# Optimization experiments

Hardware: AMD Instinct MI355X
Metric: run time of the kernel (lower is better)

Reference implementation:

```python
import jax, jax.numpy as jnp
import numpy as np


def _unfold(x, r):
    # x: [b, ch, h, w] -> [b, ch, k*k, h, w], zero-padded 3x3-style neighborhoods
    b, ch, h, w = x.shape
    k = 2 * r + 1
    xp = jnp.pad(x, ((0, 0), (0, 0), (r, r), (r, r)))
    patches = [xp[:, :, i:i + h, j:j + w] for i in range(k) for j in range(k)]
    return jnp.stack(patches, axis=2)


def setup_inputs() -> dict:
    key = jax.random.key(0)
    ks = jax.random.split(key, 6)
    b, c, h, w = 4, 128, 128, 128
    scale = 1.0 / np.sqrt(c)
    return {
        "feature0": jax.random.normal(ks[0], (b, c, h, w), jnp.float32),
        "flow": jax.random.normal(ks[1], (b, 2, h, w), jnp.float32),
        "q_w": jax.random.normal(ks[2], (c, c), jnp.float32) * scale,
        "q_b": jax.random.normal(ks[3], (c,), jnp.float32) * 0.01,
        "k_w": jax.random.normal(ks[4], (c, c), jnp.float32) * scale,
        "k_b": jax.random.normal(ks[5], (c,), jnp.float32) * 0.01,
        "local_window_attn": 1,
        "local_window_radius": 1,
    }


def reference(feature0, flow, q_w, q_b, k_w, k_b, local_window_attn, local_window_radius):
    b, c, h, w = feature0.shape
    inv_sqrt_c = 1.0 / jnp.sqrt(jnp.asarray(c, feature0.dtype))
    x = feature0.reshape(b, c, h * w).transpose(0, 2, 1)  # [b, hw, c]
    q = x @ q_w.T + q_b  # q_proj
    if local_window_attn:
        r = local_window_radius
        kf = x @ k_w.T + k_b  # k_proj applied to original feature
        kmap = kf.transpose(0, 2, 1).reshape(b, c, h, w)
        kwin = _unfold(kmap, r)      # [b, c, k2, h, w]
        fwin = _unfold(flow, r)      # [b, 2, k2, h, w]
        qmap = q.reshape(b, h, w, c)
        scores = jnp.einsum('bhwc,bckhw->bhwk', qmap, kwin) * inv_sqrt_c
        prob = jax.nn.softmax(scores, axis=-1)
        out = jnp.einsum('bhwk,bfkhw->bfhw', prob, fwin)  # [b, 2, h, w]
        return out
    else:
        # NOTE: faithful to source, key = k_proj(q_proj(x))
        key_ = q @ k_w.T + k_b
        value = flow.reshape(b, flow.shape[1], h * w).transpose(0, 2, 1)  # [b, hw, 2]
        scores = jnp.einsum('bnc,bmc->bnm', q, key_) * inv_sqrt_c
        prob = jax.nn.softmax(scores, axis=-1)
        out = jnp.einsum('bnm,bmf->bnf', prob, value)
        return out.reshape(b, h, w, value.shape[-1]).transpose(0, 3, 1, 2)
```

## Files before the change

kernel.cpp:

```cpp
#include <hip/hip_runtime.h>


#define HW 16384
#define NB 4
#define TOT (NB * HW)

typedef short bf16x8 __attribute__((ext_vector_type(8)));
typedef float f32x4 __attribute__((ext_vector_type(4)));

__device__ __forceinline__ unsigned short f2bf(float f) {
    unsigned u = __float_as_uint(f);
    return (unsigned short)((u + 0x7fffu + ((u >> 16) & 1u)) >> 16);
}
__device__ __forceinline__ float bf2f(unsigned short s) {
    return __uint_as_float(((unsigned)s) << 16);
}

__global__ void prep_kernel(const float* __restrict__ qw, const float* __restrict__ qb,
                            const float* __restrict__ kw, const float* __restrict__ kb,
                            unsigned short* __restrict__ MhT, unsigned short* __restrict__ MlT,
                            float* __restrict__ u, float* __restrict__ v,
                            float* __restrict__ dptr) {
    __shared__ float red[128];
    int bid = blockIdx.x, tid = threadIdx.x;
    if (bid < 128) {
        int ci = bid;
        int cj = tid & 127, half = tid >> 7;
        int co0 = half * 64;
        const float* kcol = kw + ci;
        float acc = 0.f;
#pragma unroll 4
        for (int co = 0; co < 64; ++co)
            acc += kcol[(size_t)(co0 + co) * 128] * qw[(size_t)(co0 + co) * 128 + cj];
        if (half) red[cj] = acc;
        __syncthreads();
        if (!half) {
            float mval = acc + red[cj];
            unsigned short h = f2bf(mval);
            MhT[ci * 128 + cj] = h;
            MlT[ci * 128 + cj] = f2bf(mval - bf2f(h));
        }
    } else {
        int half = tid >> 7, t = tid & 127;
        const float* w  = half ? kw : qw;
        const float* bv = half ? qb : kb;
        float acc = 0.f;
#pragma unroll 4
        for (int co = 0; co < 128; ++co) acc += w[co * 128 + t] * bv[co];
        if (half) v[t] = acc; else u[t] = acc;
        if (!half) red[t] = qb[t] * kb[t];
        __syncthreads();
        if (tid == 0) {
            float dd = 0.f;
            for (int i = 0; i < 128; ++i) dd += red[i];
            *dptr = dd;
        }
    }
}

__global__ __launch_bounds__(512, 4)
void fused_kernel(const float* __restrict__ feat,
                  const unsigned short* __restrict__ MhT, const unsigned short* __restrict__ MlT,
                  const float* __restrict__ u, const float* __restrict__ v,
                  const float* __restrict__ dptr, const float* __restrict__ flow,
                  float* __restrict__ out) {
    __shared__ float zbuf[16384];
    int tid = threadIdx.x;
    int bid = blockIdx.x;
    int b = bid >> 7, row = bid & 127;
    int p0 = row * 128;

    {
        char* lbase = (char*)zbuf;
#pragma unroll
        for (int it = 0; it < 4; ++it) {
            int chunk = it * 512 + tid;
            int off = chunk * 16;
            int swz = off ^ (((off >> 8) & 7) << 4);
            bf16x8 tv = *(const bf16x8*)((const char*)MhT + off);
            *(bf16x8*)(lbase + swz) = tv;
            bf16x8 tv2 = *(const bf16x8*)((const char*)MlT + off);
            *(bf16x8*)(lbase + 32768 + swz) = tv2;
        }
    }
    __syncthreads();

    {
        int wave = tid >> 6, lane = tid & 63;
        int m = lane & 15, q = lane >> 4;
        int wp0 = wave * 16;
        const float* xbase = feat + (size_t)b * 128 * HW + p0 + wp0;
        const char* lbase = (const char*)zbuf;

        f32x4 zero = {0.f, 0.f, 0.f, 0.f};
        f32x4 acc[8];
#pragma unroll
        for (int t = 0; t < 8; ++t) acc[t] = zero;

#pragma unroll
        for (int kc = 0; kc < 4; ++kc) {
            int c0 = kc * 32;
            const float* xp = xbase + (size_t)(c0 + q * 8) * HW + m;
            float xv[8];
#pragma unroll
            for (int j = 0; j < 8; ++j) xv[j] = xp[(size_t)j * HW];
            bf16x8 bh, bl;
#pragma unroll
            for (int j = 0; j < 8; ++j) {
                unsigned short hh = f2bf(xv[j]);
                bh[j] = (short)hh;
                bl[j] = (short)f2bf(xv[j] - bf2f(hh));
            }
            int colb = (c0 + q * 8) * 2;
            int swzx = ((m & 7) << 4);
#pragma unroll
            for (int t = 0; t < 8; ++t) {
                int offr = ((t * 16 + m) * 256 + colb) ^ swzx;
                bf16x8 ah = *(const bf16x8*)(lbase + offr);
                bf16x8 al = *(const bf16x8*)(lbase + 32768 + offr);
                acc[t] = __builtin_amdgcn_mfma_f32_16x16x32_bf16(ah, bh, acc[t], 0, 0, 0);
                acc[t] = __builtin_amdgcn_mfma_f32_16x16x32_bf16(ah, bl, acc[t], 0, 0, 0);
                acc[t] = __builtin_amdgcn_mfma_f32_16x16x32_bf16(al, bh, acc[t], 0, 0, 0);
            }
        }
        __syncthreads();
        int px = wp0 + (lane & 15);
        int rg = lane >> 4;
#pragma unroll
        for (int t = 0; t < 8; ++t)
#pragma unroll
            for (int r = 0; r < 4; ++r) {
                int c = t * 16 + rg * 4 + r;
                zbuf[px * 128 + ((c + px) & 127)] = acc[t][r] + v[c];
            }
    }
    __syncthreads();

    {
        int spx = tid & 127, h = tid >> 7;
        int p = p0 + spx;
        float sc[9];
#pragma unroll
        for (int k = 0; k < 9; ++k) sc[k] = 0.f;
        float g = 0.f;
#pragma unroll 2
        for (int cc = 0; cc < 32; ++cc) {
            int c = h * 32 + cc;
            float zv = zbuf[spx * 128 + ((c + spx) & 127)];
            const float* xc = feat + ((size_t)b * 128 + c) * HW;
            float xcen = 0.f;
#pragma unroll
            for (int dy = 0; dy < 3; ++dy) {
                int off = p + (dy - 1) * 128;
                int om = max(0, min(HW - 1, off - 1));
                int oc = max(0, min(HW - 1, off));
                int op = max(0, min(HW - 1, off + 1));
                float xm = xc[om], x0 = xc[oc], xp1 = xc[op];
                sc[dy * 3 + 0] += zv * xm;
                sc[dy * 3 + 1] += zv * x0;
                sc[dy * 3 + 2] += zv * xp1;
                if (dy == 1) xcen = x0;
            }
            g += u[c] * xcen;
        }
        __syncthreads();
#pragma unroll
        for (int k = 0; k < 9; ++k)
            zbuf[(k * 128 + spx) * 4 + h] = sc[k];
        zbuf[(9 * 128 + spx) * 4 + h] = g;
    }
    __syncthreads();

    if (tid < 128) {
        int spx = tid;
        int p = p0 + spx;
        int col = spx;
        const float inv = 0.08838834764831845f;
        float dconst = *dptr;
        float g = zbuf[(9 * 128 + spx) * 4 + 0] + zbuf[(9 * 128 + spx) * 4 + 1]
                + zbuf[(9 * 128 + spx) * 4 + 2] + zbuf[(9 * 128 + spx) * 4 + 3];

        float sc[9];
        float mx = -1e30f;
#pragma unroll
        for (int k = 0; k < 9; ++k) {
            int dy = k / 3 - 1, dx = (k % 3) - 1;
            float ssum = zbuf[(k * 128 + spx) * 4 + 0] + zbuf[(k * 128 + spx) * 4 + 1]
                       + zbuf[(k * 128 + spx) * 4 + 2] + zbuf[(k * 128 + spx) * 4 + 3];
            bool valid = ((unsigned)(row + dy) < 128u) && ((unsigned)(col + dx) < 128u);
            float s = valid ? (ssum + g + dconst) * inv : 0.f;
            sc[k] = s;
            mx = fmaxf(mx, s);
        }
        float e[9], sum = 0.f;
#pragma unroll
        for (int k = 0; k < 9; ++k) { e[k] = __expf(sc[k] - mx); sum += e[k]; }
        float rs = 1.f / sum;

        float o0 = 0.f, o1 = 0.f;
#pragma unroll
        for (int k = 0; k < 9; ++k) {
            int dy = k / 3 - 1, dx = (k % 3) - 1;
            bool valid = ((unsigned)(row + dy) < 128u) && ((unsigned)(col + dx) < 128u);
            float pr = valid ? e[k] * rs : 0.f;
            int poff = p + dy * 128 + dx;
            poff = max(0, min(HW - 1, poff));
            o0 += pr * flow[(size_t)(b * 2) * HW + poff];
            o1 += pr * flow[(size_t)(b * 2 + 1) * HW + poff];
        }
        out[(size_t)(b * 2) * HW + p] = o0;
        out[(size_t)(b * 2 + 1) * HW + p] = o1;
    }
}

extern "C" void kernel_launch(void* const* d_in, const int* in_sizes, int n_in,
                              void* d_out, int out_size, void* d_ws, size_t ws_size,
                              hipStream_t stream) {
    const float* feat = (const float*)d_in[0];
    const float* flow = (const float*)d_in[1];
    const float* qw = (const float*)d_in[2];
    const float* qb = (const float*)d_in[3];
    const float* kw = (const float*)d_in[4];
    const float* kb = (const float*)d_in[5];

    float* ws = (float*)d_ws;
    float* u = ws;
    float* v = ws + 128;
    float* dptr = ws + 256;
    unsigned short* MhT = (unsigned short*)(ws + 512);
    unsigned short* MlT = (unsigned short*)(ws + 8704);
    float* out = (float*)d_out;

    prep_kernel<<<129, 256, 0, stream>>>(qw, qb, kw, kb, MhT, MlT, u, v, dptr);
    fused_kernel<<<512, 512, 0, stream>>>(feat, MhT, MlT, u, v, dptr, flow, out);
}
```

Baseline: 116.6 us.

## Consume MFMA accumulators directly for window dot products, reduce via wave shuffles

```diff
diff --git a/kernel.cpp b/kernel.cpp
--- a/kernel.cpp
+++ b/kernel.cpp
@@ -64,152 +64,148 @@
                   const float* __restrict__ u, const float* __restrict__ v,
                   const float* __restrict__ dptr, const float* __restrict__ flow,
                   float* __restrict__ out) {
-    __shared__ float zbuf[16384];
+    __shared__ char lds[65536];
     int tid = threadIdx.x;
     int bid = blockIdx.x;
-    int b = bid >> 7, row = bid & 127;
+    int rowid = (bid & 7) * 64 + (bid >> 3);
+    int b = rowid >> 7, row = rowid & 127;
     int p0 = row * 128;
 
-    {
-        char* lbase = (char*)zbuf;
-#pragma unroll
-        for (int it = 0; it < 4; ++it) {
-            int chunk = it * 512 + tid;
-            int off = chunk * 16;
-            int swz = off ^ (((off >> 8) & 7) << 4);
-            bf16x8 tv = *(const bf16x8*)((const char*)MhT + off);
-            *(bf16x8*)(lbase + swz) = tv;
-            bf16x8 tv2 = *(const bf16x8*)((const char*)MlT + off);
-            *(bf16x8*)(lbase + 32768 + swz) = tv2;
-        }
+#pragma unroll
+    for (int it = 0; it < 4; ++it) {
+        int off = (it * 512 + tid) * 16;
+        int swz = off ^ (((off >> 8) & 7) << 4);
+        *(bf16x8*)(lds + swz) = *(const bf16x8*)((const char*)MhT + off);
+        *(bf16x8*)(lds + 32768 + swz) = *(const bf16x8*)((const char*)MlT + off);
     }
     __syncthreads();
 
-    {
-        int wave = tid >> 6, lane = tid & 63;
-        int m = lane & 15, q = lane >> 4;
-        int wp0 = wave * 16;
-        const float* xbase = feat + (size_t)b * 128 * HW + p0 + wp0;
-        const char* lbase = (const char*)zbuf;
-
-        f32x4 zero = {0.f, 0.f, 0.f, 0.f};
-        f32x4 acc[8];
-#pragma unroll
-        for (int t = 0; t < 8; ++t) acc[t] = zero;
-
-#pragma unroll
-        for (int kc = 0; kc < 4; ++kc) {
-            int c0 = kc * 32;
-            const float* xp = xbase + (size_t)(c0 + q * 8) * HW + m;
-            float xv[8];
-#pragma unroll
-            for (int j = 0; j < 8; ++j) xv[j] = xp[(size_t)j * HW];
-            bf16x8 bh, bl;
-#pragma unroll
-            for (int j = 0; j < 8; ++j) {
-                unsigned short hh = f2bf(xv[j]);
-                bh[j] = (short)hh;
-                bl[j] = (short)f2bf(xv[j] - bf2f(hh));
+    int wave = tid >> 6, lane = tid & 63;
+    int m = lane & 15, q = lane >> 4;
+    int col = wave * 16 + m;
+    const float* xbase = feat + (size_t)b * 128 * HW + p0 + wave * 16;
+
+    f32x4 zero = {0.f, 0.f, 0.f, 0.f};
+    f32x4 acc[8];
+#pragma unroll
+    for (int t = 0; t < 8; ++t) acc[t] = zero;
+
+#pragma unroll
+    for (int kc = 0; kc < 4; ++kc) {
+        int c0 = kc * 32;
+        const float* xp = xbase + (size_t)(c0 + q * 8) * HW + m;
+        float xv[8];
+#pragma unroll
+        for (int j = 0; j < 8; ++j) xv[j] = xp[(size_t)j * HW];
+        bf16x8 bh, bl;
+#pragma unroll
+        for (int j = 0; j < 8; ++j) {
+            unsigned short hh = f2bf(xv[j]);
+            bh[j] = (short)hh;
+            bl[j] = (short)f2bf(xv[j] - bf2f(hh));
+        }
+        int colb = (c0 + q * 8) * 2;
+        int swzx = (m & 7) << 4;
+#pragma unroll
+        for (int t = 0; t < 8; ++t) {
+            int offr = ((t * 16 + m) * 256 + colb) ^ swzx;
+            bf16x8 ah = *(const bf16x8*)(lds + offr);
+            bf16x8 al = *(const bf16x8*)(lds + 32768 + offr);
+            acc[t] = __builtin_amdgcn_mfma_f32_16x16x32_bf16(ah, bh, acc[t], 0, 0, 0);
+            acc[t] = __builtin_amdgcn_mfma_f32_16x16x32_bf16(ah, bl, acc[t], 0, 0, 0);
+            acc[t] = __builtin_amdgcn_mfma_f32_16x16x32_bf16(al, bh, acc[t], 0, 0, 0);
+        }
+    }
+#pragma unroll
+    for (int t = 0; t < 8; ++t) {
+        float4 vv = *(const float4*)(v + t * 16 + q * 4);
+#pragma unroll
+        for (int r = 0; r < 4; ++r) acc[t][r] += ((const float*)&vv)[r];
+    }
+
+    int a0 = (row > 0 ? row - 1 : 0) * 128;
+    int a1 = row * 128;
+    int a2 = (row < 127 ? row + 1 : 127) * 128;
+    int cm = col > 0 ? col - 1 : 0;
+    int cp = col < 127 ? col + 1 : 127;
+    const float* fb = feat + (size_t)b * 128 * HW;
+
+    float sc[9];
+#pragma unroll
+    for (int k = 0; k < 9; ++k) sc[k] = 0.f;
+    float g = 0.f;
+
+#pragma unroll
+    for (int t = 0; t < 8; ++t) {
+        float4 uu = *(const float4*)(u + t * 16 + q * 4);
+#pragma unroll
+        for (int r = 0; r < 4; ++r) {
+            float zv = acc[t][r];
+            const float* xc = fb + (size_t)(t * 16 + q * 4 + r) * HW;
+            {
+                const float* xr = xc + a0;
+                sc[0] += zv * xr[cm]; sc[1] += zv * xr[col]; sc[2] += zv * xr[cp];
             }
-            int colb = (c0 + q * 8) * 2;
-            int swzx = ((m & 7) << 4);
-#pragma unroll
-            for (int t = 0; t < 8; ++t) {
-                int offr = ((t * 16 + m) * 256 + colb) ^ swzx;
-                bf16x8 ah = *(const bf16x8*)(lbase + offr);
-                bf16x8 al = *(const bf16x8*)(lbase + 32768 + offr);
-                acc[t] = __builtin_amdgcn_mfma_f32_16x16x32_bf16(ah, bh, acc[t], 0, 0, 0);
-                acc[t] = __builtin_amdgcn_mfma_f32_16x16x32_bf16(ah, bl, acc[t], 0, 0, 0);
-                acc[t] = __builtin_amdgcn_mfma_f32_16x16x32_bf16(al, bh, acc[t], 0, 0, 0);
+            {
+                const float* xr = xc + a1;
+                float x0 = xr[col];
+                sc[3] += zv * xr[cm]; sc[4] += zv * x0; sc[5] += zv * xr[cp];
+                g += ((const float*)&uu)[r] * x0;
             }
-        }
-        __syncthreads();
-        int px = wp0 + (lane & 15);
-        int rg = lane >> 4;
-#pragma unroll
-        for (int t = 0; t < 8; ++t)
-#pragma unroll
-            for (int r = 0; r < 4; ++r) {
-                int c = t * 16 + rg * 4 + r;
-                zbuf[px * 128 + ((c + px) & 127)] = acc[t][r] + v[c];
+            {
+                const float* xr = xc + a2;
+                sc[6] += zv * xr[cm]; sc[7] += zv * xr[col]; sc[8] += zv * xr[cp];
             }
-    }
-    __syncthreads();
-
-    {
-        int spx = tid & 127, h = tid >> 7;
-        int p = p0 + spx;
-        float sc[9];
-#pragma unroll
-        for (int k = 0; k < 9; ++k) sc[k] = 0.f;
-        float g = 0.f;
-#pragma unroll 2
-        for (int cc = 0; cc < 32; ++cc) {
-            int c = h * 32 + cc;
-            float zv = zbuf[spx * 128 + ((c + spx) & 127)];
-            const float* xc = feat + ((size_t)b * 128 + c) * HW;
-            float xcen = 0.f;
-#pragma unroll
-            for (int dy = 0; dy < 3; ++dy) {
-                int off = p + (dy - 1) * 128;
-                int om = max(0, min(HW - 1, off - 1));
-                int oc = max(0, min(HW - 1, off));
-                int op = max(0, min(HW - 1, off + 1));
-                float xm = xc[om], x0 = xc[oc], xp1 = xc[op];
-                sc[dy * 3 + 0] += zv * xm;
-                sc[dy * 3 + 1] += zv * x0;
-                sc[dy * 3 + 2] += zv * xp1;
-                if (dy == 1) xcen = x0;
-            }
-            g += u[c] * xcen;
-        }
-        __syncthreads();
-#pragma unroll
-        for (int k = 0; k < 9; ++k)
-            zbuf[(k * 128 + spx) * 4 + h] = sc[k];
-        zbuf[(9 * 128 + spx) * 4 + h] = g;
-    }
-    __syncthreads();
-
-    if (tid < 128) {
-        int spx = tid;
-        int p = p0 + spx;
-        int col = spx;
-        const float inv = 0.08838834764831845f;
-        float dconst = *dptr;
-        float g = zbuf[(9 * 128 + spx) * 4 + 0] + zbuf[(9 * 128 + spx) * 4 + 1]
-                + zbuf[(9 * 128 + spx) * 4 + 2] + zbuf[(9 * 128 + spx) * 4 + 3];
-
-        float sc[9];
-        float mx = -1e30f;
-#pragma unroll
-        for (int k = 0; k < 9; ++k) {
-            int dy = k / 3 - 1, dx = (k % 3) - 1;
-            float ssum = zbuf[(k * 128 + spx) * 4 + 0] + zbuf[(k * 128 + spx) * 4 + 1]
-                       + zbuf[(k * 128 + spx) * 4 + 2] + zbuf[(k * 128 + spx) * 4 + 3];
-            bool valid = ((unsigned)(row + dy) < 128u) && ((unsigned)(col + dx) < 128u);
-            float s = valid ? (ssum + g + dconst) * inv : 0.f;
-            sc[k] = s;
-            mx = fmaxf(mx, s);
-        }
-        float e[9], sum = 0.f;
-#pragma unroll
-        for (int k = 0; k < 9; ++k) { e[k] = __expf(sc[k] - mx); sum += e[k]; }
-        float rs = 1.f / sum;
-
-        float o0 = 0.f, o1 = 0.f;
-#pragma unroll
-        for (int k = 0; k < 9; ++k) {
-            int dy = k / 3 - 1, dx = (k % 3) - 1;
-            bool valid = ((unsigned)(row + dy) < 128u) && ((unsigned)(col + dx) < 128u);
-            float pr = valid ? e[k] * rs : 0.f;
-            int poff = p + dy * 128 + dx;
-            poff = max(0, min(HW - 1, poff));
-            o0 += pr * flow[(size_t)(b * 2) * HW + poff];
-            o1 += pr * flow[(size_t)(b * 2 + 1) * HW + poff];
-        }
-        out[(size_t)(b * 2) * HW + p] = o0;
-        out[(size_t)(b * 2 + 1) * HW + p] = o1;
+        }
+    }
+
+#pragma unroll
+    for (int k = 0; k < 9; ++k) {
+        sc[k] += __shfl_xor(sc[k], 16);
+        sc[k] += __shfl_xor(sc[k], 32);
+    }
+    g += __shfl_xor(g, 16);
+    g += __shfl_xor(g, 32);
+
+    const float inv = 0.08838834764831845f;
+    float base = g + *dptr;
+    bool rok0 = row > 0, rok2 = row < 127;
+    bool cok0 = col > 0, cok2 = col < 127;
+    bool vmask[9] = { rok0 && cok0, rok0, rok0 && cok2,
+                      cok0,         true, cok2,
+                      rok2 && cok0, rok2, rok2 && cok2 };
+
+    float s[9];
+    float mx = -1e30f;
+#pragma unroll
+    for (int k = 0; k < 9; ++k) {
+        float sv = vmask[k] ? (sc[k] + base) * inv : 0.f;
+        s[k] = sv;
+        mx = fmaxf(mx, sv);
+    }
+    float e[9], sum = 0.f;
+#pragma unroll
+    for (int k = 0; k < 9; ++k) { e[k] = __expf(s[k] - mx); sum += e[k]; }
+    float rs = 1.f / sum;
+
+    const float* f0 = flow + (size_t)(b * 2) * HW;
+    const float* f1 = f0 + HW;
+    int av[3] = {a0, a1, a2};
+    int cv[3] = {cm, col, cp};
+    float o0 = 0.f, o1 = 0.f;
+#pragma unroll
+    for (int dy = 0; dy < 3; ++dy)
+#pragma unroll
+        for (int dx = 0; dx < 3; ++dx) {
+            int k = dy * 3 + dx;
+            float pr = vmask[k] ? e[k] * rs : 0.f;
+            int off = av[dy] + cv[dx];
+            o0 += pr * f0[off];
+            o1 += pr * f1[off];
+        }
+    if (q == 0) {
+        out[(size_t)(b * 2) * HW + p0 + col] = o0;
+        out[(size_t)(b * 2 + 1) * HW + p0 + col] = o1;
     }
 }
 
```

Result: faster. 108.5 us (median of 2 runs) (-7.0%).
